# Kernel optimization log

Hardware: AMD Instinct MI355X
Metric: run time of the kernel (lower is better)

The kernel has to match this reference:

```python
import jax, jax.numpy as jnp
import numpy as np

BN_EPS = 1e-5

def _bn_eval(x, g, b, m, v):
    # BatchNorm1d in eval mode with running stats
    return (x - m) * (g / jnp.sqrt(v + BN_EPS)) + b

def _gcn_layer(x, adj, w, b):
    # D^-0.5 A D^-0.5 (X W) + b  (same math as diag(d^-0.5) @ adj @ diag(d^-0.5))
    deg = adj.sum(axis=1)
    dis = deg ** -0.5
    xw = x @ w
    return dis[:, None] * (adj @ (dis[:, None] * xw)) + b

def setup_inputs() -> dict:
    key = jax.random.key(0)
    ks = jax.random.split(key, 8)
    N, F, E, H, G, C = 16384, 1024, 256, 256, 128, 10
    def xavier(k, i, o):
        s = float(np.sqrt(6.0 / (i + o)))
        return jax.random.uniform(k, (i, o), jnp.float32, -s, s)
    return {
        "feature": jax.random.uniform(ks[0], (N, F), jnp.float32),
        "adj": jax.random.uniform(ks[1], (N, N), jnp.float32),
        "enc_w1": xavier(ks[2], F, 512), "enc_b1": jnp.zeros((512,), jnp.float32),
        "bn1_g": jnp.ones((512,), jnp.float32), "bn1_b": jnp.zeros((512,), jnp.float32),
        "bn1_m": jnp.zeros((512,), jnp.float32), "bn1_v": jnp.ones((512,), jnp.float32),
        "enc_w2": xavier(ks[3], 512, E), "enc_b2": jnp.zeros((E,), jnp.float32),
        "bn2_g": jnp.ones((E,), jnp.float32), "bn2_b": jnp.zeros((E,), jnp.float32),
        "bn2_m": jnp.zeros((E,), jnp.float32), "bn2_v": jnp.ones((E,), jnp.float32),
        "gcn1_w": xavier(ks[4], E, H), "gcn1_b": jnp.zeros((H,), jnp.float32),
        "gcn2_w": xavier(ks[5], H, G), "gcn2_b": jnp.zeros((G,), jnp.float32),
        "cls_w": xavier(ks[6], G, C), "cls_b": jnp.zeros((C,), jnp.float32),
    }

def reference(feature, adj, enc_w1, enc_b1, bn1_g, bn1_b, bn1_m, bn1_v,
              enc_w2, enc_b2, bn2_g, bn2_b, bn2_m, bn2_v,
              gcn1_w, gcn1_b, gcn2_w, gcn2_b, cls_w, cls_b):
    # encoder.encode (eval: dropout off, BN running stats)
    h = jax.nn.relu(_bn_eval(feature @ enc_w1 + enc_b1, bn1_g, bn1_b, bn1_m, bn1_v))
    h = jax.nn.relu(_bn_eval(h @ enc_w2 + enc_b2, bn2_g, bn2_b, bn2_m, bn2_v))
    h = jax.nn.relu(_gcn_layer(h, adj, gcn1_w, gcn1_b))
    h = jax.nn.relu(_gcn_layer(h, adj, gcn2_w, gcn2_b))
    out = jax.nn.sigmoid(h @ cls_w + cls_b)
    return jnp.clip(out, 1e-10, 1 - 1e-10)
```

## Files before the change

### kernel.cpp

```cpp
#include <hip/hip_runtime.h>
#include <stdint.h>

typedef unsigned short u16;
typedef unsigned int u32;
typedef __attribute__((ext_vector_type(4))) float f32x4;
typedef __attribute__((ext_vector_type(16))) float f32x16;
typedef __attribute__((ext_vector_type(8))) short s16x8;
typedef __attribute__((ext_vector_type(4))) short s16x4;
typedef __attribute__((ext_vector_type(2))) unsigned int u32x2;
typedef __attribute__((ext_vector_type(4))) unsigned int u32x4;
typedef __attribute__((ext_vector_type(8))) int i32x8;

__device__ __forceinline__ u16 f2bf(float x){
  unsigned u = __builtin_bit_cast(unsigned, x);
  u += 0x7fffu + ((u >> 16) & 1u);
  return (u16)(u >> 16);
}
__device__ __forceinline__ float bf2f(u16 b){
  return __builtin_bit_cast(float, (unsigned)b << 16);
}
__device__ __forceinline__ u32 pk_fp8x4(float a, float b, float c, float d){
  int w = 0;
  w = __builtin_amdgcn_cvt_pk_fp8_f32(a, b, w, false);
  w = __builtin_amdgcn_cvt_pk_fp8_f32(c, d, w, true);
  return (u32)w;
}


__global__ void bn_prep_kernel(const float* __restrict__ g, const float* __restrict__ b,
                               const float* __restrict__ m, const float* __restrict__ v,
                               const float* __restrict__ lin_b,
                               float* __restrict__ s, float* __restrict__ bb, int n){
  int i = blockIdx.x * 256 + threadIdx.x;
  if (i < n){
    float sc = g[i] * rsqrtf(v[i] + 1e-5f);
    s[i] = sc;
    bb[i] = (lin_b[i] - m[i]) * sc + b[i];
  }
}

__global__ void tcvt_kernel(const float* __restrict__ src, u16* __restrict__ dst, int K, int N){
  int e = blockIdx.x * 256 + threadIdx.x;
  if (e < K * N){
    int k = e / N, n = e - k * N;
    dst[(size_t)n * K + k] = f2bf(src[e]);
  }
}

__global__ __launch_bounds__(256) void deg_kernel(const float* __restrict__ adj,
                                                  unsigned char* __restrict__ adj8,
                                                  float* __restrict__ dis, int n){
  int row = blockIdx.x;
  const float* rp = adj + (size_t)row * n;
  unsigned char* wp = adj8 + (size_t)row * n;
  float s = 0.f;
  for (int i = threadIdx.x * 8; i < n; i += 2048){
    f32x4 a = *(const f32x4*)(rp + i);
    f32x4 b = *(const f32x4*)(rp + i + 4);
    s += ((a[0] + a[1]) + (a[2] + a[3])) + ((b[0] + b[1]) + (b[2] + b[3]));
    u32x2 o;
    o[0] = pk_fp8x4(a[0], a[1], a[2], a[3]);
    o[1] = pk_fp8x4(b[0], b[1], b[2], b[3]);
    *(u32x2*)(wp + i) = o;
  }
  #pragma unroll
  for (int d = 32; d > 0; d >>= 1) s += __shfl_down(s, d, 64);
  __shared__ float ps[4];
  if ((threadIdx.x & 63) == 0) ps[threadIdx.x >> 6] = s;
  __syncthreads();
  if (threadIdx.x == 0) dis[row] = rsqrtf((ps[0] + ps[1]) + (ps[2] + ps[3]));
}

__global__ __launch_bounds__(256) void gcn_reduce_kernel(const float* __restrict__ part,
                                                         const float* __restrict__ dis,
                                                         const float* __restrict__ b,
                                                         u16* __restrict__ out,
                                                         int N, size_t MN, float oscale){
  size_t e4 = ((size_t)blockIdx.x * 256 + threadIdx.x) * 4;
  int row = (int)(e4 / N);
  int col = (int)(e4 % N);
  f32x4 s = *(const f32x4*)(part + e4);
  s += *(const f32x4*)(part + MN + e4);
  float dr = dis[row] * oscale;
  s16x4 o;
  #pragma unroll
  for (int j = 0; j < 4; j++){
    float vv = fmaxf(dr * s[j] + b[col + j], 0.f);
    o[j] = (short)f2bf(vv);
  }
  *(s16x4*)(out + e4) = o;
}

__global__ __launch_bounds__(256) void cls_kernel(const u16* __restrict__ h4,
                                                  const float* __restrict__ w,
                                                  const float* __restrict__ b,
                                                  float* __restrict__ out, int M){
  __shared__ float ws_[128 * 10];
  __shared__ float bs_[10];
  for (int i = threadIdx.x; i < 1280; i += 256) ws_[i] = w[i];
  if (threadIdx.x < 10) bs_[threadIdx.x] = b[threadIdx.x];
  __syncthreads();
  int row = blockIdx.x * 256 + threadIdx.x;
  if (row >= M) return;
  const u16* hp = h4 + (size_t)row * 128;
  float acc[10];
  #pragma unroll
  for (int c = 0; c < 10; c++) acc[c] = bs_[c];
  #pragma unroll
  for (int k8 = 0; k8 < 128; k8 += 8){
    s16x8 hv = *(const s16x8*)(hp + k8);
    #pragma unroll
    for (int j = 0; j < 8; j++){
      float h = bf2f((u16)hv[j]);
      #pragma unroll
      for (int c = 0; c < 10; c++) acc[c] = fmaf(h, ws_[(k8 + j) * 10 + c], acc[c]);
    }
  }
  #pragma unroll
  for (int c = 0; c < 10; c++){
    float sg = 1.f / (1.f + expf(-acc[c]));
    sg = fminf(fmaxf(sg, 1e-10f), 1.f - 1e-10f);
    out[(size_t)row * 10 + c] = sg;
  }
}

template<int BM, int BN>
__global__ __launch_bounds__(512, 1)
void gemm_mx(const unsigned char* __restrict__ A8, const unsigned char* __restrict__ B8,
             float* __restrict__ P, int M, int N, int K, int Ksub)
{
  constexpr int BK = 128;
  constexpr int AT = BM * BK;
  constexpr int BT = BN * BK;
  constexpr int AIT = AT / (512 * 16);
  constexpr int BIT = BT / (512 * 16);
  constexpr int WM = 2, WN = 4;
  constexpr int WTM = BM / WM;
  constexpr int WTN = BN / WN;
  constexpr int FM = WTM / 32;
  constexpr int FN = WTN / 32;
  static_assert(AIT >= 1 && BIT >= 1, "staging");

  __shared__ __align__(16) char LDS[2 * (AT + BT)];

  const int tid = threadIdx.x;
  const int lane = tid & 63;
  const int wid = tid >> 6;
  const int wr = wid >> 2;
  const int wc = wid & 3;
  const int bm = blockIdx.x * BM;
  const int kz = blockIdx.z * Ksub;

  auto stage = [&](int half, int k0){
    char* ab = LDS + half * (AT + BT);
    #pragma unroll
    for (int i = 0; i < AIT; i++){
      int e = (i * 512 + tid) * 16;
      int r = e >> 7, c = e & 127;
      int cc = c ^ ((r & 7) << 4);
      const unsigned char* g = A8 + (size_t)(bm + r) * K + k0 + cc;
      __builtin_amdgcn_global_load_lds((const __attribute__((address_space(1))) unsigned int*)g,
          (__attribute__((address_space(3))) unsigned int*)(ab + e), 16, 0, 0);
    }
    char* bb = ab + AT;
    #pragma unroll
    for (int i = 0; i < BIT; i++){
      int e = (i * 512 + tid) * 16;
      int r = e >> 7, c = e & 127;
      int cc = c ^ ((r & 7) << 4);
      const unsigned char* g = B8 + (size_t)r * K + k0 + cc;
      __builtin_amdgcn_global_load_lds((const __attribute__((address_space(1))) unsigned int*)g,
          (__attribute__((address_space(3))) unsigned int*)(bb + e), 16, 0, 0);
    }
  };

  f32x16 acc[FM][FN];
  #pragma unroll
  for (int m = 0; m < FM; m++)
    #pragma unroll
    for (int n = 0; n < FN; n++)
      #pragma unroll
      for (int i = 0; i < 16; i++)
        acc[m][n][i] = 0.f;

  const int nk = Ksub / BK;
  stage(0, kz);
  for (int kt = 0; kt < nk; ++kt){
    __syncthreads();
    if (kt + 1 < nk) stage((kt + 1) & 1, kz + (kt + 1) * BK);
    const char* ab = LDS + (kt & 1) * (AT + BT);
    const char* bb = ab + AT;
    #pragma unroll
    for (int ks = 0; ks < 2; ks++){
      const int c0 = ks * 64 + (lane >> 5) * 32;
      i32x8 af[FM], bf_[FN];
      #pragma unroll
      for (int m = 0; m < FM; m++){
        int r = wr * WTM + m * 32 + (lane & 31);
        int sw = (r & 7) << 4;
        int o = r * BK + c0;
        u32x4 lo = *(const u32x4*)(ab + (o ^ sw));
        u32x4 hi = *(const u32x4*)(ab + ((o + 16) ^ sw));
        af[m][0] = lo[0]; af[m][1] = lo[1]; af[m][2] = lo[2]; af[m][3] = lo[3];
        af[m][4] = hi[0]; af[m][5] = hi[1]; af[m][6] = hi[2]; af[m][7] = hi[3];
      }
      #pragma unroll
      for (int n = 0; n < FN; n++){
        int r = wc * WTN + n * 32 + (lane & 31);
        int sw = (r & 7) << 4;
        int o = r * BK + c0;
        u32x4 lo = *(const u32x4*)(bb + (o ^ sw));
        u32x4 hi = *(const u32x4*)(bb + ((o + 16) ^ sw));
        bf_[n][0] = lo[0]; bf_[n][1] = lo[1]; bf_[n][2] = lo[2]; bf_[n][3] = lo[3];
        bf_[n][4] = hi[0]; bf_[n][5] = hi[1]; bf_[n][6] = hi[2]; bf_[n][7] = hi[3];
      }
      #pragma unroll
      for (int m = 0; m < FM; m++)
        #pragma unroll
        for (int n = 0; n < FN; n++)
          acc[m][n] = __builtin_amdgcn_mfma_scale_f32_32x32x64_f8f6f4(
              af[m], bf_[n], acc[m][n], 0, 0, 0, 0x7F7F7F7F, 0, 0x7F7F7F7F);
    }
  }

  float* Pz = P + (size_t)blockIdx.z * M * N;
  #pragma unroll
  for (int m = 0; m < FM; m++){
    #pragma unroll
    for (int n = 0; n < FN; n++){
      int colg = wc * WTN + n * 32 + (lane & 31);
      int rbase = bm + wr * WTM + m * 32 + (lane >> 5) * 4;
      #pragma unroll
      for (int i = 0; i < 16; i++){
        int rowg = rbase + (i & 3) + 8 * (i >> 2);
        Pz[(size_t)rowg * N + colg] = acc[m][n][i];
      }
    }
  }
}

enum { EPI_BNRELU = 0, EPI_SCALET = 1 };

template<int BM, int BN, int BK, int WM, int WN, int DT, int EPI>
__global__ __launch_bounds__(WM*WN*64, 1)
void gemm_k(const void* __restrict__ Ap, const void* __restrict__ Bp,
            void* __restrict__ Cp, int M, int N, int K,
            const float* __restrict__ cs, const float* __restrict__ cb,
            const float* __restrict__ rs, float oscale)
{
  constexpr int NT = WM * WN * 64;
  constexpr int AEL = (DT == 0) ? 4 : 8;
  constexpr int WTM = BM / WM;
  constexpr int WTN = BN / WN;
  constexpr int FM = WTM / 16;
  constexpr int FN = WTN / 16;
  constexpr int AIT = (BM * BK) / (NT * AEL);
  constexpr int BIT = (BN * BK) / (NT * 8);
  static_assert((BM * BK) % (NT * AEL) == 0, "A staging");
  static_assert((BN * BK) % (NT * 8) == 0, "B staging");

  __shared__ u16 As[BM * BK];
  __shared__ u16 Bs[BN * BK];

  const int tid = threadIdx.x;
  const int lane = tid & 63;
  const int wid = tid >> 6;
  const int wr = wid / WN;
  const int wc = wid % WN;
  const int bm = blockIdx.x * BM;
  const int bn = blockIdx.y * BN;

  const float* Af = (const float*)Ap;
  const u16* Ab = (const u16*)Ap;
  const u16* Bb = (const u16*)Bp;

  f32x4 arf[DT == 0 ? AIT : 1];
  s16x8 arb[DT == 1 ? AIT : 1];
  s16x8 brb[BIT];

  auto load_tiles = [&](int k0){
    if constexpr (DT == 0){
      #pragma unroll
      for (int i = 0; i < AIT; i++){
        int e = (i * NT + tid) * 4; int r = e / BK, c = e % BK;
        arf[i] = *(const f32x4*)(Af + (size_t)(bm + r) * K + k0 + c);
      }
    } else {
      #pragma unroll
      for (int i = 0; i < AIT; i++){
        int e = (i * NT + tid) * 8; int r = e / BK, c = e % BK;
        arb[i] = *(const s16x8*)(Ab + (size_t)(bm + r) * K + k0 + c);
      }
    }
    #pragma unroll
    for (int i = 0; i < BIT; i++){
      int e = (i * NT + tid) * 8; int r = e / BK, c = e % BK;
      brb[i] = *(const s16x8*)(Bb + (size_t)(bn + r) * K + k0 + c);
    }
  };

  auto store_tiles = [&](){
    char* Ac = (char*)As; char* Bc = (char*)Bs;
    if constexpr (DT == 0){
      #pragma unroll
      for (int i = 0; i < AIT; i++){
        int e = (i * NT + tid) * 4; int r = e / BK, c = e % BK;
        int off = ((r * BK + c) * 2) ^ ((r & 7) << 4);
        s16x4 o;
        o[0] = (short)f2bf(arf[i][0]); o[1] = (short)f2bf(arf[i][1]);
        o[2] = (short)f2bf(arf[i][2]); o[3] = (short)f2bf(arf[i][3]);
        *(s16x4*)(Ac + off) = o;
      }
    } else {
      #pragma unroll
      for (int i = 0; i < AIT; i++){
        int e = (i * NT + tid) * 8; int r = e / BK, c = e % BK;
        int off = ((r * BK + c) * 2) ^ ((r & 7) << 4);
        *(s16x8*)(Ac + off) = arb[i];
      }
    }
    #pragma unroll
    for (int i = 0; i < BIT; i++){
      int e = (i * NT + tid) * 8; int r = e / BK, c = e % BK;
      int off = ((r * BK + c) * 2) ^ ((r & 7) << 4);
      *(s16x8*)(Bc + off) = brb[i];
    }
  };

  f32x4 acc[FM][FN];
  #pragma unroll
  for (int m = 0; m < FM; m++)
    #pragma unroll
    for (int n = 0; n < FN; n++)
      acc[m][n] = (f32x4){0.f, 0.f, 0.f, 0.f};

  const int arow0 = wr * WTM + (lane & 15);
  const int brow0 = wc * WTN + (lane & 15);
  const int kof = (lane >> 4) * 8;

  const int nk = K / BK;
  load_tiles(0);
  for (int kt = 0; kt < nk; ++kt){
    __syncthreads();
    store_tiles();
    __syncthreads();
    if (kt + 1 < nk) load_tiles((kt + 1) * BK);
    const char* Ac = (const char*)As;
    const char* Bc = (const char*)Bs;
    #pragma unroll
    for (int ks = 0; ks < BK / 32; ++ks){
      s16x8 af[FM], bfr[FN];
      #pragma unroll
      for (int m = 0; m < FM; m++){
        int r = arow0 + m * 16;
        af[m] = *(const s16x8*)(Ac + (((r * BK + ks * 32 + kof) * 2) ^ ((r & 7) << 4)));
      }
      #pragma unroll
      for (int n = 0; n < FN; n++){
        int r = brow0 + n * 16;
        bfr[n] = *(const s16x8*)(Bc + (((r * BK + ks * 32 + kof) * 2) ^ ((r & 7) << 4)));
      }
      #pragma unroll
      for (int m = 0; m < FM; m++)
        #pragma unroll
        for (int n = 0; n < FN; n++)
          acc[m][n] = __builtin_amdgcn_mfma_f32_16x16x32_bf16(af[m], bfr[n], acc[m][n], 0, 0, 0);
    }
  }

  #pragma unroll
  for (int m = 0; m < FM; m++){
    #pragma unroll
    for (int n = 0; n < FN; n++){
      int col = bn + wc * WTN + n * 16 + (lane & 15);
      int row0 = bm + wr * WTM + m * 16 + (lane >> 4) * 4;
      if constexpr (EPI == EPI_SCALET){
        float v0 = acc[m][n][0] * rs[row0 + 0] * oscale;
        float v1 = acc[m][n][1] * rs[row0 + 1] * oscale;
        float v2 = acc[m][n][2] * rs[row0 + 2] * oscale;
        float v3 = acc[m][n][3] * rs[row0 + 3] * oscale;
        *(u32*)((unsigned char*)Cp + (size_t)col * M + row0) = pk_fp8x4(v0, v1, v2, v3);
      } else {
        #pragma unroll
        for (int r4 = 0; r4 < 4; r4++){
          int row = row0 + r4;
          float vv = fmaxf(acc[m][n][r4] * cs[col] + cb[col], 0.f);
          ((u16*)Cp)[(size_t)row * N + col] = f2bf(vv);
        }
      }
    }
  }
}


extern "C" void kernel_launch(void* const* d_in, const int* in_sizes, int n_in,
                              void* d_out, int out_size, void* d_ws, size_t ws_size,
                              hipStream_t stream)
{
  (void)in_sizes; (void)n_in; (void)out_size; (void)ws_size;
  const float* feature = (const float*)d_in[0];
  const float* adj     = (const float*)d_in[1];
  const float* enc_w1  = (const float*)d_in[2];
  const float* enc_b1  = (const float*)d_in[3];
  const float* bn1_g   = (const float*)d_in[4];
  const float* bn1_b   = (const float*)d_in[5];
  const float* bn1_m   = (const float*)d_in[6];
  const float* bn1_v   = (const float*)d_in[7];
  const float* enc_w2  = (const float*)d_in[8];
  const float* enc_b2  = (const float*)d_in[9];
  const float* bn2_g   = (const float*)d_in[10];
  const float* bn2_b   = (const float*)d_in[11];
  const float* bn2_m   = (const float*)d_in[12];
  const float* bn2_v   = (const float*)d_in[13];
  const float* gcn1_w  = (const float*)d_in[14];
  const float* gcn1_b  = (const float*)d_in[15];
  const float* gcn2_w  = (const float*)d_in[16];
  const float* gcn2_b  = (const float*)d_in[17];
  const float* cls_w   = (const float*)d_in[18];
  const float* cls_b   = (const float*)d_in[19];
  float* out = (float*)d_out;

  const int NN = 16384, F = 1024, H1 = 512, E = 256, H = 256, G = 128;
  const float SC = 256.f, SCI = 1.f / 256.f;

  char* ws = (char*)d_ws;
  size_t off = 0;
  auto alloc = [&](size_t bytes) -> char* {
    char* p = ws + off; off += (bytes + 255) & ~(size_t)255; return p;
  };
  float* dis = (float*)alloc((size_t)NN * 4);
  float* s1  = (float*)alloc((size_t)H1 * 4);
  float* bb1 = (float*)alloc((size_t)H1 * 4);
  float* s2  = (float*)alloc((size_t)E * 4);
  float* bb2 = (float*)alloc((size_t)E * 4);
  u16* w1t = (u16*)alloc((size_t)H1 * F * 2);
  u16* w2t = (u16*)alloc((size_t)E * H1 * 2);
  u16* g1t = (u16*)alloc((size_t)H * E * 2);
  u16* g2t = (u16*)alloc((size_t)G * H * 2);
  u16* h1  = (u16*)alloc((size_t)NN * H1 * 2);
  u16* h2  = (u16*)alloc((size_t)NN * E * 2);
  unsigned char* tT  = (unsigned char*)alloc((size_t)E * NN);
  u16* h3  = (u16*)alloc((size_t)NN * H * 2);
  unsigned char* t2T = (unsigned char*)alloc((size_t)G * NN);
  u16* h4  = (u16*)alloc((size_t)NN * G * 2);
  float* part = (float*)alloc((size_t)2 * NN * H * 4);
  unsigned char* adj8 = (unsigned char*)alloc((size_t)NN * NN);

  bn_prep_kernel<<<(H1 + 255) / 256, 256, 0, stream>>>(bn1_g, bn1_b, bn1_m, bn1_v, enc_b1, s1, bb1, H1);
  bn_prep_kernel<<<(E + 255) / 256, 256, 0, stream>>>(bn2_g, bn2_b, bn2_m, bn2_v, enc_b2, s2, bb2, E);
  tcvt_kernel<<<(F * H1 + 255) / 256, 256, 0, stream>>>(enc_w1, w1t, F, H1);
  tcvt_kernel<<<(H1 * E + 255) / 256, 256, 0, stream>>>(enc_w2, w2t, H1, E);
  tcvt_kernel<<<(E * H + 255) / 256, 256, 0, stream>>>(gcn1_w, g1t, E, H);
  tcvt_kernel<<<(H * G + 255) / 256, 256, 0, stream>>>(gcn2_w, g2t, H, G);

  deg_kernel<<<NN, 256, 0, stream>>>(adj, adj8, dis, NN);

  gemm_k<128,256,64,1,4,0,EPI_BNRELU><<<dim3(NN/128, H1/256), 256, 0, stream>>>(
      feature, w1t, h1, NN, H1, F, s1, bb1, nullptr, 1.f);
  gemm_k<128,128,64,2,2,1,EPI_BNRELU><<<dim3(NN/128, E/128), 256, 0, stream>>>(
      h1, w2t, h2, NN, E, H1, s2, bb2, nullptr, 1.f);
  gemm_k<128,128,64,2,2,1,EPI_SCALET><<<dim3(NN/128, H/128), 256, 0, stream>>>(
      h2, g1t, tT, NN, H, E, nullptr, nullptr, dis, SC);
  gemm_mx<128,256><<<dim3(NN/128, 1, 2), 512, 0, stream>>>(
      adj8, tT, part, NN, H, NN, NN/2);
  gcn_reduce_kernel<<<(NN * H) / 1024, 256, 0, stream>>>(
      part, dis, gcn1_b, h3, H, (size_t)NN * H, SCI);
  gemm_k<128,128,64,2,2,1,EPI_SCALET><<<dim3(NN/128, G/128), 256, 0, stream>>>(
      h3, g2t, t2T, NN, G, H, nullptr, nullptr, dis, SC);
  gemm_mx<128,128><<<dim3(NN/128, 1, 2), 512, 0, stream>>>(
      adj8, t2T, part, NN, G, NN, NN/2);
  gcn_reduce_kernel<<<(NN * G) / 1024, 256, 0, stream>>>(
      part, dis, gcn2_b, h4, G, (size_t)NN * G, SCI);
  cls_kernel<<<NN/256, 256, 0, stream>>>(h4, cls_w, cls_b, out, NN);
}
```

Baseline: 555.2 us.

## Fuse encoder GEMM1 with adjacency degree/fp8 pass and tile weight transposes

Merges the first encoder GEMM and the adjacency degree/fp8 conversion into one launch, where the first 256 blocks run the GEMM and the remaining blocks each process one adj row. The aim is to overlap the compute-heavy GEMM with the bandwidth-heavy adj pass. Weight transposes now use a shared-memory tiled kernel so both reads and writes are coalesced. The gcn2 projection GEMM uses a smaller BM tile to launch more blocks. The fused kernel hardcodes the problem sizes, and its GEMM uses a different warp layout (2x2) than the old 1x4 launch.

```diff
diff --git a/kernel.cpp b/kernel.cpp
--- a/kernel.cpp
+++ b/kernel.cpp
@@ -39,36 +39,158 @@
   }
 }
 
-__global__ void tcvt_kernel(const float* __restrict__ src, u16* __restrict__ dst, int K, int N){
-  int e = blockIdx.x * 256 + threadIdx.x;
-  if (e < K * N){
-    int k = e / N, n = e - k * N;
-    dst[(size_t)n * K + k] = f2bf(src[e]);
-  }
-}
-
-__global__ __launch_bounds__(256) void deg_kernel(const float* __restrict__ adj,
-                                                  unsigned char* __restrict__ adj8,
-                                                  float* __restrict__ dis, int n){
-  int row = blockIdx.x;
-  const float* rp = adj + (size_t)row * n;
-  unsigned char* wp = adj8 + (size_t)row * n;
-  float s = 0.f;
-  for (int i = threadIdx.x * 8; i < n; i += 2048){
-    f32x4 a = *(const f32x4*)(rp + i);
-    f32x4 b = *(const f32x4*)(rp + i + 4);
-    s += ((a[0] + a[1]) + (a[2] + a[3])) + ((b[0] + b[1]) + (b[2] + b[3]));
-    u32x2 o;
-    o[0] = pk_fp8x4(a[0], a[1], a[2], a[3]);
-    o[1] = pk_fp8x4(b[0], b[1], b[2], b[3]);
-    *(u32x2*)(wp + i) = o;
-  }
-  #pragma unroll
-  for (int d = 32; d > 0; d >>= 1) s += __shfl_down(s, d, 64);
-  __shared__ float ps[4];
-  if ((threadIdx.x & 63) == 0) ps[threadIdx.x >> 6] = s;
+__global__ __launch_bounds__(256) void tcvtT_kernel(const float* __restrict__ src,
+                                                    u16* __restrict__ dst, int K, int N){
+  __shared__ float t[32][33];
+  int tx = threadIdx.x & 31, ty = threadIdx.x >> 5;
+  int n0 = blockIdx.x * 32, k0 = blockIdx.y * 32;
+  #pragma unroll
+  for (int i = 0; i < 4; i++)
+    t[ty + 8 * i][tx] = src[(size_t)(k0 + ty + 8 * i) * N + n0 + tx];
   __syncthreads();
-  if (threadIdx.x == 0) dis[row] = rsqrtf((ps[0] + ps[1]) + (ps[2] + ps[3]));
+  #pragma unroll
+  for (int i = 0; i < 4; i++)
+    dst[(size_t)(n0 + ty + 8 * i) * K + k0 + tx] = f2bf(t[tx][ty + 8 * i]);
+}
+
+__global__ __launch_bounds__(256) void enc1_deg_kernel(
+    const float* __restrict__ feature, const u16* __restrict__ w1t,
+    u16* __restrict__ h1, const float* __restrict__ cs, const float* __restrict__ cb,
+    const float* __restrict__ adj, unsigned char* __restrict__ adj8,
+    float* __restrict__ dis)
+{
+  constexpr int BM = 128, BN = 256, BK = 64, WM = 2, WN = 2;
+  constexpr int M = 16384, N = 512, K = 1024, NADJ = 16384;
+  constexpr int WTM = BM / WM, WTN = BN / WN, FM = WTM / 16, FN = WTN / 16;
+  constexpr int AIT = (BM * BK) / (256 * 4);
+  constexpr int BIT = (BN * BK) / (256 * 8);
+
+  __shared__ __align__(16) char smem[BM * BK * 2 + BN * BK * 2];
+
+  if (blockIdx.x >= 256){
+    int row = blockIdx.x - 256;
+    const float* rp = adj + (size_t)row * NADJ;
+    unsigned char* wp = adj8 + (size_t)row * NADJ;
+    float s = 0.f;
+    #pragma unroll
+    for (int it = 0; it < 4; ++it){
+      const float* p = rp + it * 4096 + threadIdx.x * 16;
+      f32x4 v[4];
+      #pragma unroll
+      for (int j = 0; j < 4; ++j) v[j] = *(const f32x4*)(p + 4 * j);
+      u32x4 o;
+      #pragma unroll
+      for (int j = 0; j < 4; ++j){
+        s += (v[j][0] + v[j][1]) + (v[j][2] + v[j][3]);
+        o[j] = pk_fp8x4(v[j][0], v[j][1], v[j][2], v[j][3]);
+      }
+      *(u32x4*)(wp + it * 4096 + threadIdx.x * 16) = o;
+    }
+    #pragma unroll
+    for (int d = 32; d > 0; d >>= 1) s += __shfl_down(s, d, 64);
+    float* ps = (float*)smem;
+    if ((threadIdx.x & 63) == 0) ps[threadIdx.x >> 6] = s;
+    __syncthreads();
+    if (threadIdx.x == 0) dis[row] = rsqrtf((ps[0] + ps[1]) + (ps[2] + ps[3]));
+    return;
+  }
+
+  u16* As = (u16*)smem;
+  u16* Bs = (u16*)(smem + BM * BK * 2);
+  const int tid = threadIdx.x;
+  const int lane = tid & 63;
+  const int wid = tid >> 6;
+  const int wr = wid / WN;
+  const int wc = wid % WN;
+  const int bm = (blockIdx.x & 127) * BM;
+  const int bn = (blockIdx.x >> 7) * BN;
+
+  f32x4 arf[AIT];
+  s16x8 brb[BIT];
+
+  auto load_tiles = [&](int k0){
+    #pragma unroll
+    for (int i = 0; i < AIT; i++){
+      int e = (i * 256 + tid) * 4; int r = e / BK, c = e % BK;
+      arf[i] = *(const f32x4*)(feature + (size_t)(bm + r) * K + k0 + c);
+    }
+    #pragma unroll
+    for (int i = 0; i < BIT; i++){
+      int e = (i * 256 + tid) * 8; int r = e / BK, c = e % BK;
+      brb[i] = *(const s16x8*)(w1t + (size_t)(bn + r) * K + k0 + c);
+    }
+  };
+  auto store_tiles = [&](){
+    char* Ac = (char*)As; char* Bc = (char*)Bs;
+    #pragma unroll
+    for (int i = 0; i < AIT; i++){
+      int e = (i * 256 + tid) * 4; int r = e / BK, c = e % BK;
+      int off = ((r * BK + c) * 2) ^ ((r & 7) << 4);
+      s16x4 o;
+      o[0] = (short)f2bf(arf[i][0]); o[1] = (short)f2bf(arf[i][1]);
+      o[2] = (short)f2bf(arf[i][2]); o[3] = (short)f2bf(arf[i][3]);
+      *(s16x4*)(Ac + off) = o;
+    }
+    #pragma unroll
+    for (int i = 0; i < BIT; i++){
+      int e = (i * 256 + tid) * 8; int r = e / BK, c = e % BK;
+      int off = ((r * BK + c) * 2) ^ ((r & 7) << 4);
+      *(s16x8*)(Bc + off) = brb[i];
+    }
+  };
+
+  f32x4 acc[FM][FN];
+  #pragma unroll
+  for (int m = 0; m < FM; m++)
+    #pragma unroll
+    for (int n = 0; n < FN; n++)
+      acc[m][n] = (f32x4){0.f, 0.f, 0.f, 0.f};
+
+  const int arow0 = wr * WTM + (lane & 15);
+  const int brow0 = wc * WTN + (lane & 15);
+  const int kof = (lane >> 4) * 8;
+
+  load_tiles(0);
+  for (int kt = 0; kt < K / BK; ++kt){
+    __syncthreads();
+    store_tiles();
+    __syncthreads();
+    if (kt + 1 < K / BK) load_tiles((kt + 1) * BK);
+    const char* Ac = (const char*)As;
+    const char* Bc = (const char*)Bs;
+    #pragma unroll
+    for (int ks = 0; ks < BK / 32; ++ks){
+      s16x8 af[FM], bfr[FN];
+      #pragma unroll
+      for (int m = 0; m < FM; m++){
+        int r = arow0 + m * 16;
+        af[m] = *(const s16x8*)(Ac + (((r * BK + ks * 32 + kof) * 2) ^ ((r & 7) << 4)));
+      }
+      #pragma unroll
+      for (int n = 0; n < FN; n++){
+        int r = brow0 + n * 16;
+        bfr[n] = *(const s16x8*)(Bc + (((r * BK + ks * 32 + kof) * 2) ^ ((r & 7) << 4)));
+      }
+      #pragma unroll
+      for (int m = 0; m < FM; m++)
+        #pragma unroll
+        for (int n = 0; n < FN; n++)
+          acc[m][n] = __builtin_amdgcn_mfma_f32_16x16x32_bf16(af[m], bfr[n], acc[m][n], 0, 0, 0);
+    }
+  }
+  #pragma unroll
+  for (int m = 0; m < FM; m++){
+    #pragma unroll
+    for (int n = 0; n < FN; n++){
+      int col = bn + wc * WTN + n * 16 + (lane & 15);
+      int row0 = bm + wr * WTM + m * 16 + (lane >> 4) * 4;
+      #pragma unroll
+      for (int r4 = 0; r4 < 4; r4++){
+        float vv = fmaxf(acc[m][n][r4] * cs[col] + cb[col], 0.f);
+        h1[(size_t)(row0 + r4) * N + col] = f2bf(vv);
+      }
+    }
+  }
 }
 
 __global__ __launch_bounds__(256) void gcn_reduce_kernel(const float* __restrict__ part,
@@ -241,22 +363,21 @@
 
 enum { EPI_BNRELU = 0, EPI_SCALET = 1 };
 
-template<int BM, int BN, int BK, int WM, int WN, int DT, int EPI>
+template<int BM, int BN, int BK, int WM, int WN, int EPI>
 __global__ __launch_bounds__(WM*WN*64, 1)
-void gemm_k(const void* __restrict__ Ap, const void* __restrict__ Bp,
+void gemm_k(const u16* __restrict__ Ab, const u16* __restrict__ Bb,
             void* __restrict__ Cp, int M, int N, int K,
             const float* __restrict__ cs, const float* __restrict__ cb,
             const float* __restrict__ rs, float oscale)
 {
   constexpr int NT = WM * WN * 64;
-  constexpr int AEL = (DT == 0) ? 4 : 8;
   constexpr int WTM = BM / WM;
   constexpr int WTN = BN / WN;
   constexpr int FM = WTM / 16;
   constexpr int FN = WTN / 16;
-  constexpr int AIT = (BM * BK) / (NT * AEL);
+  constexpr int AIT = (BM * BK) / (NT * 8);
   constexpr int BIT = (BN * BK) / (NT * 8);
-  static_assert((BM * BK) % (NT * AEL) == 0, "A staging");
+  static_assert((BM * BK) % (NT * 8) == 0, "A staging");
   static_assert((BN * BK) % (NT * 8) == 0, "B staging");
 
   __shared__ u16 As[BM * BK];
@@ -270,27 +391,14 @@
   const int bm = blockIdx.x * BM;
   const int bn = blockIdx.y * BN;
 
-  const float* Af = (const float*)Ap;
-  const u16* Ab = (const u16*)Ap;
-  const u16* Bb = (const u16*)Bp;
-
-  f32x4 arf[DT == 0 ? AIT : 1];
-  s16x8 arb[DT == 1 ? AIT : 1];
+  s16x8 arb[AIT];
   s16x8 brb[BIT];
 
   auto load_tiles = [&](int k0){
-    if constexpr (DT == 0){
-      #pragma unroll
-      for (int i = 0; i < AIT; i++){
-        int e = (i * NT + tid) * 4; int r = e / BK, c = e % BK;
-        arf[i] = *(const f32x4*)(Af + (size_t)(bm + r) * K + k0 + c);
-      }
-    } else {
-      #pragma unroll
-      for (int i = 0; i < AIT; i++){
-        int e = (i * NT + tid) * 8; int r = e / BK, c = e % BK;
-        arb[i] = *(const s16x8*)(Ab + (size_t)(bm + r) * K + k0 + c);
-      }
+    #pragma unroll
+    for (int i = 0; i < AIT; i++){
+      int e = (i * NT + tid) * 8; int r = e / BK, c = e % BK;
+      arb[i] = *(const s16x8*)(Ab + (size_t)(bm + r) * K + k0 + c);
     }
     #pragma unroll
     for (int i = 0; i < BIT; i++){
@@ -298,26 +406,13 @@
       brb[i] = *(const s16x8*)(Bb + (size_t)(bn + r) * K + k0 + c);
     }
   };
-
   auto store_tiles = [&](){
     char* Ac = (char*)As; char* Bc = (char*)Bs;
-    if constexpr (DT == 0){
-      #pragma unroll
-      for (int i = 0; i < AIT; i++){
-        int e = (i * NT + tid) * 4; int r = e / BK, c = e % BK;
-        int off = ((r * BK + c) * 2) ^ ((r & 7) << 4);
-        s16x4 o;
-        o[0] = (short)f2bf(arf[i][0]); o[1] = (short)f2bf(arf[i][1]);
-        o[2] = (short)f2bf(arf[i][2]); o[3] = (short)f2bf(arf[i][3]);
-        *(s16x4*)(Ac + off) = o;
-      }
-    } else {
-      #pragma unroll
-      for (int i = 0; i < AIT; i++){
-        int e = (i * NT + tid) * 8; int r = e / BK, c = e % BK;
-        int off = ((r * BK + c) * 2) ^ ((r & 7) << 4);
-        *(s16x8*)(Ac + off) = arb[i];
-      }
+    #pragma unroll
+    for (int i = 0; i < AIT; i++){
+      int e = (i * NT + tid) * 8; int r = e / BK, c = e % BK;
+      int off = ((r * BK + c) * 2) ^ ((r & 7) << 4);
+      *(s16x8*)(Ac + off) = arb[i];
     }
     #pragma unroll
     for (int i = 0; i < BIT; i++){
@@ -448,24 +543,22 @@
 
   bn_prep_kernel<<<(H1 + 255) / 256, 256, 0, stream>>>(bn1_g, bn1_b, bn1_m, bn1_v, enc_b1, s1, bb1, H1);
   bn_prep_kernel<<<(E + 255) / 256, 256, 0, stream>>>(bn2_g, bn2_b, bn2_m, bn2_v, enc_b2, s2, bb2, E);
-  tcvt_kernel<<<(F * H1 + 255) / 256, 256, 0, stream>>>(enc_w1, w1t, F, H1);
-  tcvt_kernel<<<(H1 * E + 255) / 256, 256, 0, stream>>>(enc_w2, w2t, H1, E);
-  tcvt_kernel<<<(E * H + 255) / 256, 256, 0, stream>>>(gcn1_w, g1t, E, H);
-  tcvt_kernel<<<(H * G + 255) / 256, 256, 0, stream>>>(gcn2_w, g2t, H, G);
-
-  deg_kernel<<<NN, 256, 0, stream>>>(adj, adj8, dis, NN);
-
-  gemm_k<128,256,64,1,4,0,EPI_BNRELU><<<dim3(NN/128, H1/256), 256, 0, stream>>>(
-      feature, w1t, h1, NN, H1, F, s1, bb1, nullptr, 1.f);
-  gemm_k<128,128,64,2,2,1,EPI_BNRELU><<<dim3(NN/128, E/128), 256, 0, stream>>>(
+  tcvtT_kernel<<<dim3(H1/32, F/32), 256, 0, stream>>>(enc_w1, w1t, F, H1);
+  tcvtT_kernel<<<dim3(E/32, H1/32), 256, 0, stream>>>(enc_w2, w2t, H1, E);
+  tcvtT_kernel<<<dim3(H/32, E/32), 256, 0, stream>>>(gcn1_w, g1t, E, H);
+  tcvtT_kernel<<<dim3(G/32, H/32), 256, 0, stream>>>(gcn2_w, g2t, H, G);
+
+  enc1_deg_kernel<<<256 + NN, 256, 0, stream>>>(feature, w1t, h1, s1, bb1, adj, adj8, dis);
+
+  gemm_k<128,128,64,2,2,EPI_BNRELU><<<dim3(NN/128, E/128), 256, 0, stream>>>(
       h1, w2t, h2, NN, E, H1, s2, bb2, nullptr, 1.f);
-  gemm_k<128,128,64,2,2,1,EPI_SCALET><<<dim3(NN/128, H/128), 256, 0, stream>>>(
+  gemm_k<128,128,64,2,2,EPI_SCALET><<<dim3(NN/128, H/128), 256, 0, stream>>>(
       h2, g1t, tT, NN, H, E, nullptr, nullptr, dis, SC);
   gemm_mx<128,256><<<dim3(NN/128, 1, 2), 512, 0, stream>>>(
       adj8, tT, part, NN, H, NN, NN/2);
   gcn_reduce_kernel<<<(NN * H) / 1024, 256, 0, stream>>>(
       part, dis, gcn1_b, h3, H, (size_t)NN * H, SCI);
-  gemm_k<128,128,64,2,2,1,EPI_SCALET><<<dim3(NN/128, G/128), 256, 0, stream>>>(
+  gemm_k<64,128,64,2,2,EPI_SCALET><<<dim3(NN/64, G/128), 256, 0, stream>>>(
       h3, g2t, t2T, NN, G, H, nullptr, nullptr, dis, SC);
   gemm_mx<128,128><<<dim3(NN/128, 1, 2), 512, 0, stream>>>(
       adj8, t2T, part, NN, G, NN, NN/2);
```

Result: faster. 520.4 us (-6.3%).
